# Performance work log

Measured on AMD Instinct MI355X. Metric: run time of the kernel, lower is better.

Reference implementation:

```python
import jax, jax.numpy as jnp
import numpy as np

B, C, M, T = 2, 512, 16, 128
H = 8
D = C // H  # 64, divisible by 4 for 2D RoPE
G = C // 4  # GroupNorm groups = 128
S = M * T


def group_norm(x, scale, bias, groups=G, eps=1e-5):
    b, c, m, t = x.shape
    xg = x.reshape(b, groups, c // groups, m, t)
    mu = xg.mean(axis=(2, 3, 4), keepdims=True)
    var = xg.var(axis=(2, 3, 4), keepdims=True)
    xn = ((xg - mu) * jax.lax.rsqrt(var + eps)).reshape(b, c, m, t)
    return xn * scale[None, :, None, None] + bias[None, :, None, None]


def dwsep_conv(x, dw, pw):
    # depthwise 3x3 (groups=C) then pointwise 1x1
    y = jax.lax.conv_general_dilated(
        x, dw, window_strides=(1, 1), padding='SAME',
        dimension_numbers=('NCHW', 'HWIO', 'NCHW'), feature_group_count=x.shape[1])
    return jnp.einsum('bcmt,cd->bdmt', y, pw)


def rope2d(x):
    # x: [B,H,M,T,D]; first D/2 dims rotated by freq index m, last D/2 by time index t
    d = x.shape[-1]
    dh = d // 2
    q = dh // 2
    inv = 1.0 / (10000.0 ** (jnp.arange(q, dtype=jnp.float32) / q))

    def rot(v, ang):
        h = v.shape[-1] // 2
        v1, v2 = v[..., :h], v[..., h:]
        c, s = jnp.cos(ang), jnp.sin(ang)
        return jnp.concatenate([v1 * c - v2 * s, v1 * s + v2 * c], axis=-1)

    ang_f = jnp.arange(x.shape[2], dtype=jnp.float32)[:, None] * inv  # [M,q]
    ang_t = jnp.arange(x.shape[3], dtype=jnp.float32)[:, None] * inv  # [T,q]
    xf = rot(x[..., :dh], ang_f[:, None, :])  # broadcast over T
    xt = rot(x[..., dh:], ang_t)
    return jnp.concatenate([xf, xt], axis=-1)


def setup_inputs() -> dict:
    key = jax.random.key(0)
    ks = jax.random.split(key, 14)
    s = 0.02
    return {
        'x': jax.random.normal(ks[0], (B, C, M, T), jnp.float32),
        'lengths': jax.random.randint(ks[1], (B,), T // 2, T + 1),
        'gn_scale': jnp.ones((C,), jnp.float32),
        'gn_bias': jnp.zeros((C,), jnp.float32),
        'dw_q': jax.random.normal(ks[2], (3, 3, 1, C), jnp.float32) * s,
        'dw_k': jax.random.normal(ks[3], (3, 3, 1, C), jnp.float32) * s,
        'dw_v': jax.random.normal(ks[4], (3, 3, 1, C), jnp.float32) * s,
        'pw_q': jax.random.normal(ks[5], (C, C), jnp.float32) * s,
        'pw_k': jax.random.normal(ks[6], (C, C), jnp.float32) * s,
        'pw_v': jax.random.normal(ks[7], (C, C), jnp.float32) * s,
        'attn_w': jax.random.normal(ks[8], (C, C), jnp.float32) * s,
        'attn_b': jnp.zeros((C,), jnp.float32),
        'out_w': jax.random.normal(ks[9], (C, C), jnp.float32) * s,
        'out_b': jnp.zeros((C,), jnp.float32),
    }


def reference(x, lengths, gn_scale, gn_bias, dw_q, dw_k, dw_v, pw_q, pw_k, pw_v,
              attn_w, attn_b, out_w, out_b):
    residual = x
    xn = group_norm(x, gn_scale, gn_bias)

    def to_heads(y):  # [B,C,M,T] -> [B,H,M,T,D]
        return y.reshape(B, H, D, M, T).transpose(0, 1, 3, 4, 2)

    q = rope2d(to_heads(dwsep_conv(xn, dw_q, pw_q)))
    k = rope2d(to_heads(dwsep_conv(xn, dw_k, pw_k)))
    v = to_heads(dwsep_conv(xn, dw_v, pw_v))

    q = q.reshape(B, H, S, D)
    k = k.reshape(B, H, S, D)
    v = v.reshape(B, H, S, D)

    scores = jnp.einsum('bhsd,bhkd->bhsk', q, k) / np.sqrt(D).astype(np.float32)
    valid_t = jnp.arange(T)[None, :] < lengths[:, None]        # [B,T]
    valid = jnp.tile(valid_t, (1, M))                          # [B,S], token idx = m*T + t
    scores = jnp.where(valid[:, None, None, :], scores, jnp.float32(-1e9))
    attn = jax.nn.softmax(scores, axis=-1)
    o = jnp.einsum('bhsk,bhkd->bhsd', attn, v)                 # [B,H,S,D]

    o = o.transpose(0, 2, 1, 3).reshape(B, S, C)
    o = o @ attn_w + attn_b                                    # block output proj
    o = o.reshape(B, M, T, C).transpose(0, 3, 1, 2)            # [B,C,M,T]
    out = jnp.einsum('bcmt,cd->bdmt', o, out_w) + out_b[None, :, None, None]
    return residual + out
```

## Files before the change

### kernel.cpp

```cpp
#include <hip/hip_runtime.h>
#include <math.h>

#define CCH 512
#define SSQ 2048
#define MTOT 4096

typedef __bf16 bf16;
typedef __bf16 bf16x8 __attribute__((ext_vector_type(8)));
typedef __bf16 bf16x4 __attribute__((ext_vector_type(4)));
typedef float  f32x4  __attribute__((ext_vector_type(4)));

#define AS1 __attribute__((address_space(1)))
#define AS3 __attribute__((address_space(3)))
__device__ __forceinline__ void glds16(const void* g, void* l) {
    __builtin_amdgcn_global_load_lds((const AS1 void*)g, (AS3 void*)l, 16, 0, 0);
}

__global__ __launch_bounds__(256) void gnw_kernel(const float* __restrict__ x,
        float* __restrict__ mu, float* __restrict__ rstd,
        const float* __restrict__ w0, const float* __restrict__ w1,
        const float* __restrict__ w2, const float* __restrict__ w3,
        const float* __restrict__ w4, bf16* __restrict__ wT,
        const float* __restrict__ attnb, const float* __restrict__ outb,
        float* __restrict__ bcv) {
    __shared__ float smem[64*65];
    int tid = threadIdx.x;
    if (blockIdx.x < 256) {
        float* s_sum = smem;
        float* s_sq  = smem + 256;
        int bg = blockIdx.x;
        long base = (long)bg * 8192;
        float sum = 0.f, sq = 0.f;
#pragma unroll
        for (int r = 0; r < 32; ++r) {
            float v = x[base + r*256 + tid];
            sum += v; sq += v*v;
        }
        s_sum[tid] = sum; s_sq[tid] = sq;
        __syncthreads();
        for (int off = 128; off > 0; off >>= 1) {
            if (tid < off) { s_sum[tid] += s_sum[tid+off]; s_sq[tid] += s_sq[tid+off]; }
            __syncthreads();
        }
        if (tid == 0) {
            float m = s_sum[0] * (1.f/8192.f);
            float v = s_sq[0]  * (1.f/8192.f) - m*m;
            mu[bg] = m;
            rstd[bg] = rsqrtf(v + 1e-5f);
        }
    } else if (blockIdx.x < 576) {
        int bid = blockIdx.x - 256;
        int z = bid >> 6, r2 = bid & 63;
        int k0 = (r2 >> 3)*64, n0 = (r2 & 7)*64;
        const float* srcs[5] = {w0, w1, w2, w3, w4};
        const float* W = srcs[z];
        bf16* D = wT + (long)z * (CCH*CCH);
        float (*t)[65] = (float(*)[65])smem;
        int cI = tid & 63, r4 = tid >> 6;
#pragma unroll
        for (int p = 0; p < 16; ++p) {
            int kr = p*4 + r4;
            t[kr][cI] = W[(long)(k0+kr)*CCH + n0 + cI];
        }
        __syncthreads();
#pragma unroll
        for (int p = 0; p < 16; ++p) {
            int nr = p*4 + r4;
            D[(long)(n0+nr)*CCH + k0 + cI] = (bf16)t[cI][nr];
        }
    } else if (blockIdx.x < 578) {
        int n = (blockIdx.x - 576)*256 + tid;
        float a = outb[n];
#pragma unroll 16
        for (int j = 0; j < 512; ++j)
            a = fmaf(attnb[j], w4[(long)j*CCH + n], a);
        bcv[n] = a;
    } else {
        bf16* wAc = wT + (long)5*CCH*CCH;
        int base = (blockIdx.x - 578)*4096 + tid;
#pragma unroll
        for (int p = 0; p < 16; ++p)
            wAc[base + p*256] = (bf16)w3[base + p*256];
    }
}

__global__ void tn_kernel(const float* __restrict__ x, const float* __restrict__ mu,
                          const float* __restrict__ rstd, const float* __restrict__ gsc,
                          const float* __restrict__ gbs, bf16* __restrict__ xnT) {
    __shared__ float t[64][65];
    int s0 = blockIdx.x*64, c0 = blockIdx.y*64, b = blockIdx.z;
    int tid = threadIdx.x;
    int cI = tid & 63, r4 = tid >> 6;
#pragma unroll
    for (int p = 0; p < 16; ++p) {
        int cr = p*4 + r4;
        t[cr][cI] = x[((long)(b*CCH + c0 + cr))*SSQ + s0 + cI];
    }
    __syncthreads();
#pragma unroll
    for (int p = 0; p < 16; ++p) {
        int sr = p*4 + r4;
        int c = c0 + cI;
        int g = b*128 + (c >> 2);
        float v = (t[cI][sr] - mu[g]) * rstd[g] * gsc[c] + gbs[c];
        xnT[((long)(b*SSQ + s0 + sr))*CCH + c] = (bf16)v;
    }
}

__global__ __launch_bounds__(256) void dw3_kernel(const bf16* __restrict__ xnT,
        const float* __restrict__ dwq, const float* __restrict__ dwk,
        const float* __restrict__ dwv,
        bf16* __restrict__ yq, bf16* __restrict__ yk, bf16* __restrict__ yv) {
    int tid = threadIdx.x;
    int cc = (tid & 63) * 8;
    int s  = blockIdx.x*4 + (tid >> 6);
    int sl = s & (SSQ-1);
    int b  = s >> 11;
    int m = sl >> 7, t = sl & 127;
    float aq[8] = {}, ak[8] = {}, av[8] = {};
#pragma unroll
    for (int di = 0; di < 3; ++di) {
        int m2 = m + di - 1;
        if ((unsigned)m2 >= 16u) continue;
#pragma unroll
        for (int dj = 0; dj < 3; ++dj) {
            int t2 = t + dj - 1;
            if ((unsigned)t2 >= 128u) continue;
            bf16x8 xv = *(const bf16x8*)(xnT + ((long)(b*SSQ + m2*128 + t2))*CCH + cc);
            int wi = (di*3 + dj)*CCH + cc;
#pragma unroll
            for (int i = 0; i < 8; ++i) {
                float xf = (float)xv[i];
                aq[i] += xf * dwq[wi+i];
                ak[i] += xf * dwk[wi+i];
                av[i] += xf * dwv[wi+i];
            }
        }
    }
    bf16x8 oq, ok, ov;
#pragma unroll
    for (int i = 0; i < 8; ++i) { oq[i] = (bf16)aq[i]; ok[i] = (bf16)ak[i]; ov[i] = (bf16)av[i]; }
    long o = (long)s*CCH + cc;
    *(bf16x8*)(yq + o) = oq;
    *(bf16x8*)(yk + o) = ok;
    *(bf16x8*)(yv + o) = ov;
}

template<int NFR>
__device__ __forceinline__ void gemm_core128(const bf16* __restrict__ A,
        const bf16* __restrict__ Wt, int m0, int n0,
        bf16* As, bf16* Bs, f32x4 (&acc)[4][NFR]) {
    int tid = threadIdx.x, lane = tid & 63, wid = tid >> 6;
    int sw = wid & 1, nw = wid >> 1;
    int col = lane & 15, quad = lane >> 4;
    const char* gA[4]; char* ldsA[4];
#pragma unroll
    for (int p = 0; p < 4; ++p) {
        int ci = tid + p*256;
        int row = ci >> 3;
        int c = (ci & 7) ^ (row & 7);
        gA[p] = (const char*)A + ((long)(m0+row)*CCH + c*8)*2;
        ldsA[p] = (char*)As + ci*16;
    }
    const char* gB[NFR]; char* ldsB[NFR];
#pragma unroll
    for (int p = 0; p < NFR; ++p) {
        int ci = tid + p*256;
        int row = ci >> 3;
        int c = (ci & 7) ^ (row & 7);
        gB[p] = (const char*)Wt + ((long)(n0+row)*CCH + c*8)*2;
        ldsB[p] = (char*)Bs + ci*16;
    }
    int rowA = sw*64 + col;
    int rowB = nw*(NFR*16) + col;
    for (int k0 = 0; k0 < CCH; k0 += 64) {
        __syncthreads();
#pragma unroll
        for (int p = 0; p < 4; ++p)   glds16(gA[p] + k0*2, ldsA[p]);
#pragma unroll
        for (int p = 0; p < NFR; ++p) glds16(gB[p] + k0*2, ldsB[p]);
        __syncthreads();
        bf16x8 af[4][2], bfr[NFR][2];
#pragma unroll
        for (int mt = 0; mt < 4; ++mt) {
            int r = rowA + mt*16;
#pragma unroll
            for (int ks = 0; ks < 2; ++ks) {
                int c = (ks*4 + quad) ^ (r & 7);
                af[mt][ks] = *(const bf16x8*)((char*)As + r*128 + c*16);
            }
        }
#pragma unroll
        for (int nt = 0; nt < NFR; ++nt) {
            int r = rowB + nt*16;
#pragma unroll
            for (int ks = 0; ks < 2; ++ks) {
                int c = (ks*4 + quad) ^ (r & 7);
                bfr[nt][ks] = *(const bf16x8*)((char*)Bs + r*128 + c*16);
            }
        }
#pragma unroll
        for (int ks = 0; ks < 2; ++ks)
#pragma unroll
            for (int mt = 0; mt < 4; ++mt)
#pragma unroll
                for (int nt = 0; nt < NFR; ++nt)
                    acc[mt][nt] = __builtin_amdgcn_mfma_f32_16x16x32_bf16(
                        af[mt][ks], bfr[nt][ks], acc[mt][nt], 0,0,0);
    }
}

__global__ __launch_bounds__(256) void gemm_qkv(const bf16* __restrict__ Abase,
        bf16* __restrict__ wT, bf16* __restrict__ qout,
        bf16* __restrict__ kout, bf16* __restrict__ vout) {
    __shared__ bf16 As[128*64];
    __shared__ bf16 Bs[64*64];
    int z = blockIdx.z;
    if (z == 3 && blockIdx.x >= 4) return;
    int m0 = blockIdx.x*128, n0 = blockIdx.y*64;
    const bf16* Aop = (z < 3) ? Abase + (long)z*MTOT*CCH : wT + (long)4*CCH*CCH;
    const bf16* Wop = (z < 3) ? wT + (long)z*CCH*CCH   : wT + (long)5*CCH*CCH;
    f32x4 acc[4][2] = {};
    gemm_core128<2>(Aop, Wop, m0, n0, As, Bs, acc);
    int tid = threadIdx.x, lane = tid & 63, wid = tid >> 6;
    int sw = wid & 1, nw = wid >> 1;
    int col = lane & 15, quad = lane >> 4;
    int nb = n0 + nw*32, mb = m0 + sw*64;
    if (z == 3) {
        bf16* wCt = wT + (long)6*CCH*CCH;
#pragma unroll
        for (int nt = 0; nt < 2; ++nt) {
            int n = nb + nt*16 + col;
#pragma unroll
            for (int mt = 0; mt < 4; ++mt)
#pragma unroll
                for (int r = 0; r < 4; ++r)
                    wCt[(long)(mb + mt*16 + quad*4 + r)*CCH + n] = (bf16)acc[mt][nt][r];
        }
    } else if (z < 2) {
        bf16* outp = z ? kout : qout;
        const float sc = z ? 1.0f : 0.125f;
        float invf = __expf(-(float)col * 0.5756462732485114f);
        bool tHalf = (nb & 32) != 0;
#pragma unroll
        for (int mt = 0; mt < 4; ++mt)
#pragma unroll
            for (int r = 0; r < 4; ++r) {
                int row = mb + mt*16 + quad*4 + r;
                int sl = row & (SSQ-1);
                float pos = tHalf ? (float)(sl & 127) : (float)(sl >> 7);
                float ang = pos * invf;
                float sn, cs;
                __sincosf(ang, &sn, &cs);
                float x1 = acc[mt][0][r], x2 = acc[mt][1][r];
                outp[(long)row*CCH + nb + col]      = (bf16)((x1*cs - x2*sn)*sc);
                outp[(long)row*CCH + nb + 16 + col] = (bf16)((x1*sn + x2*cs)*sc);
            }
    } else {
#pragma unroll
        for (int mt = 0; mt < 4; ++mt)
#pragma unroll
            for (int nt = 0; nt < 2; ++nt) {
                int n = nb + nt*16 + col;
                int row0 = mb + mt*16 + quad*4;
                int bq = row0 >> 11, sl0 = row0 & (SSQ-1);
                int sub16 = (sl0 >> 4) & 1;
                long slp = (long)(sl0 & ~31) + quad*8 + sub16*4;
                bf16x4 pk;
#pragma unroll
                for (int r = 0; r < 4; ++r) pk[r] = (bf16)acc[mt][nt][r];
                *(bf16x4*)(vout + ((long)(bq*CCH + n))*SSQ + slp) = pk;
            }
    }
}

__global__ __launch_bounds__(256) void gemm_out(const bf16* __restrict__ A,
        const bf16* __restrict__ Wt, const float* __restrict__ bias,
        const float* __restrict__ resid, float* __restrict__ outp) {
    __shared__ bf16 As[128*64];
    __shared__ bf16 Bs[64*64];
    int m0 = blockIdx.x*128, n0 = blockIdx.y*64;
    f32x4 acc[4][2] = {};
    gemm_core128<2>(A, Wt, m0, n0, As, Bs, acc);
    int tid = threadIdx.x, lane = tid & 63, wid = tid >> 6;
    int sw = wid & 1, nw = wid >> 1;
    int col = lane & 15, quad = lane >> 4;
    int nb = n0 + nw*32, mb = m0 + sw*64;
#pragma unroll
    for (int mt = 0; mt < 4; ++mt)
#pragma unroll
        for (int nt = 0; nt < 2; ++nt) {
            int n = nb + nt*16 + col;
            float bv = bias[n];
            int row0 = mb + mt*16 + quad*4;
            int b = row0 >> 11, sl0 = row0 & (SSQ-1);
            long off = ((long)(b*CCH + n))*SSQ + sl0;
            float4 rr = *(const float4*)(resid + off);
            float4 o4;
            o4.x = acc[mt][nt][0] + bv + rr.x;
            o4.y = acc[mt][nt][1] + bv + rr.y;
            o4.z = acc[mt][nt][2] + bv + rr.z;
            o4.w = acc[mt][nt][3] + bv + rr.w;
            *(float4*)(outp + off) = o4;
        }
}

__global__ __launch_bounds__(256, 2) void attn_kernel(
        const bf16* __restrict__ qb, const bf16* __restrict__ kb,
        const bf16* __restrict__ vb, const int* __restrict__ lengths,
        bf16* __restrict__ o) {
    __shared__ char KVs[2][32768];
    __shared__ float Lsm[4][4][16];
    int bid = blockIdx.x;
    int bh = bid & 15, qtb = bid >> 4;
    int b = bh >> 3, h = bh & 7;
    int tid = threadIdx.x, wid = tid >> 6, lane = tid & 63;
    int col = lane & 15, quad = lane >> 4;
    int q0 = qtb*64;
    int lenb = lengths[b];
    int thr = lenb - wid*32 - quad*4;

    const char* gp[8]; int ldsoff[8];
#pragma unroll
    for (int p = 0; p < 8; ++p) {
        int idx = p*256 + tid;
        if (p < 4) {
            int r = idx >> 3;
            int csrc = (idx & 7) ^ (r & 7);
            gp[p] = (const char*)kb + ((long)(b*SSQ + r))*1024 + h*128 + csrc*16;
        } else {
            int rem = idx & 1023;
            int r = rem >> 4;
            int csrc = (rem & 15) ^ (r & 15);
            gp[p] = (const char*)vb + ((long)(b*CCH + h*64 + r))*4096 + csrc*16;
        }
        ldsoff[p] = idx*16;
    }

    const bf16* qp = qb + (long)(b*SSQ)*CCH + h*64;
    bf16x8 qf[4][2];
#pragma unroll
    for (int qt = 0; qt < 4; ++qt)
#pragma unroll
        for (int dc = 0; dc < 2; ++dc)
            qf[qt][dc] = *(const bf16x8*)(qp + (long)(q0 + qt*16 + col)*CCH + dc*32 + quad*8);

    f32x4 of[4][4] = {};
    float ls[4] = {};
    int cswz7 = col & 7;
    int kc0 = (quad ^ cswz7)*16;
    int kc1 = ((4 + quad) ^ cswz7)*16;
    int vaddr = col*256 + (((wid*4 + quad) ^ col) & 15)*16;

#pragma unroll
    for (int p = 0; p < 8; ++p) glds16(gp[p], KVs[0] + ldsoff[p]);
    __syncthreads();

    for (int t = 0; t < 16; ++t) {
        if (t < 15) {
#pragma unroll
            for (int p = 0; p < 8; ++p) {
                const long step = (p < 4) ? 131072L : 256L;
                glds16(gp[p] + (long)(t+1)*step, KVs[(t+1) & 1] + ldsoff[p]);
            }
        }
        const char* K = KVs[t & 1] + wid*4096;
        const char* V = KVs[t & 1] + 16384;
        f32x4 sc[2][4];
#pragma unroll
        for (int sub = 0; sub < 2; ++sub) {
            f32x4 m;
#pragma unroll
            for (int r = 0; r < 4; ++r) m[r] = (sub*16 + r < thr) ? 0.f : -10000.f;
#pragma unroll
            for (int qt = 0; qt < 4; ++qt) sc[sub][qt] = m;
        }
        __builtin_amdgcn_s_setprio(1);
#pragma unroll
        for (int sub = 0; sub < 2; ++sub) {
            bf16x8 kf0 = *(const bf16x8*)(K + sub*2048 + col*128 + kc0);
            bf16x8 kf1 = *(const bf16x8*)(K + sub*2048 + col*128 + kc1);
#pragma unroll
            for (int qt = 0; qt < 4; ++qt) {
                sc[sub][qt] = __builtin_amdgcn_mfma_f32_16x16x32_bf16(kf0, qf[qt][0], sc[sub][qt], 0,0,0);
                sc[sub][qt] = __builtin_amdgcn_mfma_f32_16x16x32_bf16(kf1, qf[qt][1], sc[sub][qt], 0,0,0);
            }
        }
        __builtin_amdgcn_s_setprio(0);
        bf16x8 pf[4];
#pragma unroll
        for (int qt = 0; qt < 4; ++qt) {
            float s = 0.f;
#pragma unroll
            for (int r = 0; r < 4; ++r) {
                float e0 = __expf(sc[0][qt][r]);
                float e1 = __expf(sc[1][qt][r]);
                pf[qt][r]     = (bf16)e0;
                pf[qt][4 + r] = (bf16)e1;
                s += e0 + e1;
            }
            ls[qt] += s;
        }
        __builtin_amdgcn_s_setprio(1);
#pragma unroll
        for (int dt = 0; dt < 4; ++dt) {
            bf16x8 vf = *(const bf16x8*)(V + dt*4096 + vaddr);
#pragma unroll
            for (int qt = 0; qt < 4; ++qt)
                of[qt][dt] = __builtin_amdgcn_mfma_f32_16x16x32_bf16(pf[qt], vf, of[qt][dt], 0,0,0);
        }
        __builtin_amdgcn_s_setprio(0);
        __syncthreads();
    }

#pragma unroll
    for (int qt = 0; qt < 4; ++qt) {
        ls[qt] += __shfl_xor(ls[qt], 16);
        ls[qt] += __shfl_xor(ls[qt], 32);
    }
    float* Om = (float*)KVs;
#pragma unroll
    for (int qt = 0; qt < 4; ++qt)
#pragma unroll
        for (int dt = 0; dt < 4; ++dt)
#pragma unroll
            for (int r = 0; r < 4; ++r)
                Om[(wid*64 + qt*16 + quad*4 + r)*64 + dt*16 + col] = of[qt][dt][r];
    if (quad == 0)
#pragma unroll
        for (int qt = 0; qt < 4; ++qt) Lsm[wid][qt][col] = ls[qt];
    __syncthreads();
    bf16* ob = o + (long)(b*SSQ + q0)*CCH + h*64;
#pragma unroll
    for (int i = 0; i < 16; ++i) {
        int rr = wid*16 + i;
        float v = Om[rr*64 + lane] + Om[(64 + rr)*64 + lane]
                + Om[(128 + rr)*64 + lane] + Om[(192 + rr)*64 + lane];
        float l = Lsm[0][wid][i] + Lsm[1][wid][i] + Lsm[2][wid][i] + Lsm[3][wid][i];
        ob[(long)rr*CCH + lane] = (bf16)(v / l);
    }
}

extern "C" void kernel_launch(void* const* d_in, const int* in_sizes, int n_in,
                              void* d_out, int out_size, void* d_ws, size_t ws_size,
                              hipStream_t stream) {
    const float* x        = (const float*)d_in[0];
    const int*   lengths  = (const int*)  d_in[1];
    const float* gn_scale = (const float*)d_in[2];
    const float* gn_bias  = (const float*)d_in[3];
    const float* dw_q     = (const float*)d_in[4];
    const float* dw_k     = (const float*)d_in[5];
    const float* dw_v     = (const float*)d_in[6];
    const float* pw_q     = (const float*)d_in[7];
    const float* pw_k     = (const float*)d_in[8];
    const float* pw_v     = (const float*)d_in[9];
    const float* attn_w   = (const float*)d_in[10];
    const float* attn_b   = (const float*)d_in[11];
    const float* out_w    = (const float*)d_in[12];
    const float* out_b    = (const float*)d_in[13];
    float* out = (float*)d_out;

    char* w = (char*)d_ws;
    float* mu   = (float*)w;
    float* rstd = (float*)(w + 1024);
    float* bcv  = (float*)(w + 2048);
    bf16* wT    = (bf16*)(w + 4096);
    bf16* wCt = wT + (long)6*CCH*CCH;
    bf16* xnT  = (bf16*)(w + 0x00400000);
    bf16* yT   = (bf16*)(w + 0x00800000);
    bf16* qbf  = (bf16*)(w + 0x01400000);
    bf16* kbf  = (bf16*)(w + 0x01800000);
    bf16* vbf  = (bf16*)(w + 0x01C00000);
    bf16* obf  = (bf16*)(w + 0x02000000);

    gnw_kernel<<<642, 256, 0, stream>>>(x, mu, rstd, pw_q, pw_k, pw_v, attn_w, out_w,
                                        wT, attn_b, out_b, bcv);
    tn_kernel<<<dim3(32,8,2), 256, 0, stream>>>(x, mu, rstd, gn_scale, gn_bias, xnT);
    dw3_kernel<<<MTOT/4, 256, 0, stream>>>(xnT, dw_q, dw_k, dw_v,
                                           yT, yT + (long)MTOT*CCH, yT + (long)2*MTOT*CCH);

    gemm_qkv<<<dim3(MTOT/128, CCH/64, 4), 256, 0, stream>>>(yT, wT, qbf, kbf, vbf);

    attn_kernel<<<512, 256, 0, stream>>>(qbf, kbf, vbf, lengths, obf);

    gemm_out<<<dim3(MTOT/128, CCH/64), 256, 0, stream>>>(obf, wCt, bcv, x, out);
}
```

Measured before the change: 163.8 us.

## Make attention K/V tiles wave-private to drop per-iteration block barriers

```diff
diff --git a/kernel.cpp b/kernel.cpp
--- a/kernel.cpp
+++ b/kernel.cpp
@@ -320,22 +320,18 @@
     int lenb = lengths[b];
     int thr = lenb - wid*32 - quad*4;
 
-    const char* gp[8]; int ldsoff[8];
-#pragma unroll
-    for (int p = 0; p < 8; ++p) {
-        int idx = p*256 + tid;
-        if (p < 4) {
-            int r = idx >> 3;
-            int csrc = (idx & 7) ^ (r & 7);
-            gp[p] = (const char*)kb + ((long)(b*SSQ + r))*1024 + h*128 + csrc*16;
-        } else {
-            int rem = idx & 1023;
-            int r = rem >> 4;
-            int csrc = (rem & 15) ^ (r & 15);
-            gp[p] = (const char*)vb + ((long)(b*CCH + h*64 + r))*4096 + csrc*16;
-        }
-        ldsoff[p] = idx*16;
-    }
+    const char* gK[4]; const char* gV[4];
+#pragma unroll
+    for (int j = 0; j < 4; ++j) {
+        int s = j*64 + lane;
+        int rl = s >> 3;
+        int cin = s & 7;
+        int csrc = cin ^ (rl & 7);
+        gK[j] = (const char*)kb + ((long)(b*SSQ + wid*32 + rl))*1024 + h*128 + csrc*16;
+        gV[j] = (const char*)vb + ((long)(b*CCH + h*64 + j*16 + col))*4096 + (wid*4 + quad)*16;
+    }
+    char* ldsK = (char*)KVs + wid*4096 + lane*16;
+    char* ldsV = (char*)KVs + 16384 + wid*4096 + lane*16;
 
     const bf16* qp = qb + (long)(b*SSQ)*CCH + h*64;
     bf16x8 qf[4][2];
@@ -350,22 +346,41 @@
     int cswz7 = col & 7;
     int kc0 = (quad ^ cswz7)*16;
     int kc1 = ((4 + quad) ^ cswz7)*16;
-    int vaddr = col*256 + (((wid*4 + quad) ^ col) & 15)*16;
-
-#pragma unroll
-    for (int p = 0; p < 8; ++p) glds16(gp[p], KVs[0] + ldsoff[p]);
-    __syncthreads();
+
+#pragma unroll
+    for (int j = 0; j < 4; ++j) glds16(gK[j], ldsK + j*1024);
+#pragma unroll
+    for (int j = 0; j < 4; ++j) glds16(gV[j], ldsV + j*1024);
+#pragma unroll
+    for (int j = 0; j < 4; ++j) glds16(gK[j] + 131072L, ldsK + 32768 + j*1024);
+#pragma unroll
+    for (int j = 0; j < 4; ++j) glds16(gV[j] + 256L, ldsV + 32768 + j*1024);
 
     for (int t = 0; t < 16; ++t) {
-        if (t < 15) {
-#pragma unroll
-            for (int p = 0; p < 8; ++p) {
-                const long step = (p < 4) ? 131072L : 256L;
-                glds16(gp[p] + (long)(t+1)*step, KVs[(t+1) & 1] + ldsoff[p]);
-            }
-        }
+        if (t == 15) { asm volatile("s_waitcnt vmcnt(0)" ::: "memory"); }
+        else         { asm volatile("s_waitcnt vmcnt(8)" ::: "memory"); }
+        __builtin_amdgcn_sched_barrier(0);
         const char* K = KVs[t & 1] + wid*4096;
-        const char* V = KVs[t & 1] + 16384;
+        const char* V = KVs[t & 1] + 16384 + wid*4096;
+        bf16x8 kf[2][2], vf[4];
+#pragma unroll
+        for (int sub = 0; sub < 2; ++sub) {
+            kf[sub][0] = *(const bf16x8*)(K + sub*2048 + col*128 + kc0);
+            kf[sub][1] = *(const bf16x8*)(K + sub*2048 + col*128 + kc1);
+        }
+#pragma unroll
+        for (int dt = 0; dt < 4; ++dt)
+            vf[dt] = *(const bf16x8*)(V + dt*1024 + lane*16);
+        asm volatile("s_waitcnt lgkmcnt(0)" ::: "memory");
+        __builtin_amdgcn_sched_barrier(0);
+        if (t < 14) {
+            int bsel = (t & 1)*32768;
+#pragma unroll
+            for (int j = 0; j < 4; ++j) glds16(gK[j] + (long)(t+2)*131072, ldsK + bsel + j*1024);
+#pragma unroll
+            for (int j = 0; j < 4; ++j) glds16(gV[j] + (long)(t+2)*256,    ldsV + bsel + j*1024);
+        }
+        __builtin_amdgcn_sched_barrier(0);
         f32x4 sc[2][4];
 #pragma unroll
         for (int sub = 0; sub < 2; ++sub) {
@@ -377,15 +392,12 @@
         }
         __builtin_amdgcn_s_setprio(1);
 #pragma unroll
-        for (int sub = 0; sub < 2; ++sub) {
-            bf16x8 kf0 = *(const bf16x8*)(K + sub*2048 + col*128 + kc0);
-            bf16x8 kf1 = *(const bf16x8*)(K + sub*2048 + col*128 + kc1);
+        for (int sub = 0; sub < 2; ++sub)
 #pragma unroll
             for (int qt = 0; qt < 4; ++qt) {
-                sc[sub][qt] = __builtin_amdgcn_mfma_f32_16x16x32_bf16(kf0, qf[qt][0], sc[sub][qt], 0,0,0);
-                sc[sub][qt] = __builtin_amdgcn_mfma_f32_16x16x32_bf16(kf1, qf[qt][1], sc[sub][qt], 0,0,0);
-            }
-        }
+                sc[sub][qt] = __builtin_amdgcn_mfma_f32_16x16x32_bf16(kf[sub][0], qf[qt][0], sc[sub][qt], 0,0,0);
+                sc[sub][qt] = __builtin_amdgcn_mfma_f32_16x16x32_bf16(kf[sub][1], qf[qt][1], sc[sub][qt], 0,0,0);
+            }
         __builtin_amdgcn_s_setprio(0);
         bf16x8 pf[4];
 #pragma unroll
@@ -403,14 +415,11 @@
         }
         __builtin_amdgcn_s_setprio(1);
 #pragma unroll
-        for (int dt = 0; dt < 4; ++dt) {
-            bf16x8 vf = *(const bf16x8*)(V + dt*4096 + vaddr);
+        for (int dt = 0; dt < 4; ++dt)
 #pragma unroll
             for (int qt = 0; qt < 4; ++qt)
-                of[qt][dt] = __builtin_amdgcn_mfma_f32_16x16x32_bf16(pf[qt], vf, of[qt][dt], 0,0,0);
-        }
+                of[qt][dt] = __builtin_amdgcn_mfma_f32_16x16x32_bf16(pf[qt], vf[dt], of[qt][dt], 0,0,0);
         __builtin_amdgcn_s_setprio(0);
-        __syncthreads();
     }
 
 #pragma unroll
@@ -418,6 +427,7 @@
         ls[qt] += __shfl_xor(ls[qt], 16);
         ls[qt] += __shfl_xor(ls[qt], 32);
     }
+    __syncthreads();
     float* Om = (float*)KVs;
 #pragma unroll
     for (int qt = 0; qt < 4; ++qt)
```

New measurement: 162.1 us. No clear change (-1.0%).
